# Kernel tuning notes

Measured on AMD Instinct MI355X. Metric: run time of the kernel, lower is better.

Reference implementation:

```python
import jax, jax.numpy as jnp
import numpy as np

D_MODEL = 1024
NUM_HEADS = 16
D_K = D_MODEL // NUM_HEADS
NEG_INF = -1e9


def setup_inputs() -> dict:
    key = jax.random.key(0)
    ks = jax.random.split(key, 9)
    B, S, D = 4, 2048, D_MODEL
    scale = 1.0 / np.sqrt(D)
    inp = {
        "x": jax.random.normal(ks[0], (B, S, D), dtype=jnp.float32),
        "Wq": jax.random.normal(ks[1], (D, D), dtype=jnp.float32) * scale,
        "bq": jnp.zeros((D,), dtype=jnp.float32),
        "Wk": jax.random.normal(ks[2], (D, D), dtype=jnp.float32) * scale,
        "bk": jnp.zeros((D,), dtype=jnp.float32),
        "Wv": jax.random.normal(ks[3], (D, D), dtype=jnp.float32) * scale,
        "bv": jnp.zeros((D,), dtype=jnp.float32),
        "Wo": jax.random.normal(ks[4], (D, D), dtype=jnp.float32) * scale,
        "bo": jnp.zeros((D,), dtype=jnp.float32),
    }
    return inp


def reference(x, Wq, bq, Wk, bk, Wv, bv, Wo, bo):
    B, S, D = x.shape
    H, dk = NUM_HEADS, D_K
    # padding mask: token is pad if any feature == 0; shape [B,1,1,S] (keys)
    mask = (x == 0).any(axis=-1)[:, None, None, :]

    def split_heads(t):  # [B,S,D] -> [B,H,S,dk]
        return t.reshape(B, S, H, dk).transpose(0, 2, 1, 3)

    q = split_heads(x @ Wq + bq)
    k = split_heads(x @ Wk + bk)
    v = split_heads(x @ Wv + bv)

    scores = jnp.einsum("bhqd,bhkd->bhqk", q, k) / np.sqrt(dk).astype(x.dtype)
    scores = jnp.where(mask, jnp.asarray(NEG_INF, x.dtype), scores)
    weights = jax.nn.softmax(scores, axis=-1)
    context = jnp.einsum("bhqk,bhkd->bhqd", weights, v)
    context = context.transpose(0, 2, 1, 3).reshape(B, S, D)
    return context @ Wo + bo
```

## Files before the change

### kernel.cpp

```cpp
#include <hip/hip_runtime.h>
#include <cstdint>
#include <cstddef>

static constexpr int Bz = 4, S = 2048, Dm = 1024, H = 16, DK = 64;
static constexpr int M = Bz * S;

typedef __attribute__((ext_vector_type(8))) short bf16x8;
typedef __attribute__((ext_vector_type(4))) float f32x4;

__device__ __forceinline__ unsigned short f2b(float f) {
    unsigned u = __float_as_uint(f);
    return (unsigned short)((u + 0x7FFFu + ((u >> 16) & 1u)) >> 16);
}

__device__ __forceinline__ unsigned cvtpk(float lo, float hi) {
    unsigned r;
    asm("v_cvt_pk_bf16_f32 %0, %1, %2" : "=v"(r) : "v"(lo), "v"(hi));
    return r;
}

__device__ __forceinline__ float fexp2(float x) {
#if __has_builtin(__builtin_amdgcn_exp2f)
    return __builtin_amdgcn_exp2f(x);
#else
    float r;
    asm("v_exp_f32 %0, %1" : "=v"(r) : "v"(x));
    return r;
#endif
}

__device__ __forceinline__ void gld_lds16(const void* g, void* l) {
    __builtin_amdgcn_global_load_lds(
        (const __attribute__((address_space(1))) unsigned int*)g,
        (__attribute__((address_space(3))) unsigned int*)l, 16, 0, 0);
}

__global__ __launch_bounds__(256) void k_conv(const float* __restrict__ x,
                                              const float* __restrict__ Wq, const float* __restrict__ Wk,
                                              const float* __restrict__ Wv, const float* __restrict__ Wo,
                                              unsigned short* __restrict__ xb,
                                              unsigned char* __restrict__ mask,
                                              unsigned short* __restrict__ Wt) {
    const int bid = blockIdx.x;
    const int tid = threadIdx.x;
    if (bid < M) {
        const int row = bid;
        const float4 v = *(const float4*)(x + (size_t)row * Dm + tid * 4);
        const bool z = (v.x == 0.f) | (v.y == 0.f) | (v.z == 0.f) | (v.w == 0.f);
        ushort4 o;
        o.x = f2b(v.x); o.y = f2b(v.y); o.z = f2b(v.z); o.w = f2b(v.w);
        *(ushort4*)(xb + (size_t)row * Dm + tid * 4) = o;
        __shared__ int zf;
        if (tid == 0) zf = 0;
        __syncthreads();
        if (z) zf = 1;
        __syncthreads();
        if (tid == 0) mask[row] = (unsigned char)zf;
    } else {
        const int wb = bid - M;
        const int zidx = wb >> 10;
        const int rem = wb & 1023;
        const int k0 = (rem & 31) * 32, n0 = (rem >> 5) * 32;
        const float* W = (zidx == 0) ? Wq : (zidx == 1) ? Wk : (zidx == 2) ? Wv : Wo;
        unsigned short* o = Wt + (size_t)zidx * Dm * Dm;
        __shared__ float tile[32][33];
        const int tx = tid & 31, ty = tid >> 5;
#pragma unroll
        for (int i = 0; i < 4; i++)
            tile[ty + 8 * i][tx] = W[(size_t)(k0 + ty + 8 * i) * Dm + n0 + tx];
        __syncthreads();
#pragma unroll
        for (int i = 0; i < 4; i++)
            o[(size_t)(n0 + ty + 8 * i) * Dm + k0 + tx] = f2b(tile[tx][ty + 8 * i]);
    }
}

template <int MODE>
__global__ __launch_bounds__(256) void k_gemm(
    const unsigned short* __restrict__ A,
    const unsigned short* __restrict__ Bw,
    const float* __restrict__ bias0, const float* __restrict__ bias1, const float* __restrict__ bias2,
    unsigned short* __restrict__ Qo, unsigned short* __restrict__ Ko,
    unsigned short* __restrict__ Vto, float* __restrict__ Co)
{
    __shared__ unsigned short sA[128 * 64];
    __shared__ unsigned short sB[128 * 64];
    const int m0 = blockIdx.x * 128;
    const int gn0 = blockIdx.y * 128;
    const int tid = threadIdx.x;
    const int lane = tid & 63;
    const int wid = tid >> 6;
    const int wm = wid & 1, wn = wid >> 1;
    const int lr = lane & 15;
    const int lg = lane >> 4;
    f32x4 acc[4][4] = {};
    const int csrc = ((lane & 7) ^ (lane >> 3)) << 4;
    const char* gA = (const char*)A + (size_t)(m0 + (tid >> 3)) * (Dm * 2) + csrc;
    const char* gB = (const char*)Bw + (size_t)(gn0 + (tid >> 3)) * (Dm * 2) + csrc;
    for (int k0 = 0; k0 < Dm; k0 += 64) {
        __syncthreads();
#pragma unroll
        for (int j = 0; j < 4; j++) {
            gld_lds16(gA + (size_t)(j * 32) * (Dm * 2) + k0 * 2, sA + j * 2048 + wid * 512);
            gld_lds16(gB + (size_t)(j * 32) * (Dm * 2) + k0 * 2, sB + j * 2048 + wid * 512);
        }
        __syncthreads();
#pragma unroll
        for (int h = 0; h < 2; h++) {
            bf16x8 af[4], bg[4];
#pragma unroll
            for (int mi = 0; mi < 4; mi++) {
                const int row = wm * 64 + mi * 16 + lr;
                af[mi] = *(const bf16x8*)((const char*)sA + row * 128 +
                                          (((h * 4 + lg) ^ (lr & 7)) << 4));
            }
#pragma unroll
            for (int ni = 0; ni < 4; ni++) {
                const int row = wn * 64 + ni * 16 + lr;
                bg[ni] = *(const bf16x8*)((const char*)sB + row * 128 +
                                          (((h * 4 + lg) ^ (lr & 7)) << 4));
            }
#pragma unroll
            for (int mi = 0; mi < 4; mi++)
#pragma unroll
                for (int ni = 0; ni < 4; ni++)
                    acc[mi][ni] = __builtin_amdgcn_mfma_f32_16x16x32_bf16(af[mi], bg[ni], acc[mi][ni], 0, 0, 0);
        }
    }
#pragma unroll
    for (int mi = 0; mi < 4; mi++) {
        const int row0 = m0 + wm * 64 + mi * 16 + lg * 4;
#pragma unroll
        for (int ni = 0; ni < 4; ni++) {
            const int gn = gn0 + wn * 64 + ni * 16 + lr;
            const int t = gn >> 10;
            const int n = gn & 1023;
            const int h = n >> 6, d = n & 63;
            const float bsv = (MODE == 0)
                ? ((t == 0) ? bias0[n] : (t == 1) ? bias1[n] : bias2[n])
                : bias0[gn];
#pragma unroll
            for (int r = 0; r < 4; r++) {
                const int row = row0 + r;
                const float v = acc[mi][ni][r] + bsv;
                if (MODE == 0) {
                    const int bb = row >> 11;
                    const int s = row & (S - 1);
                    const size_t bh = (size_t)bb * H + h;
                    if (t == 0) {
                        Qo[(bh * S + s) * DK + d] = f2b(v * 0.18033688011f);
                    } else if (t == 1) {
                        Ko[(bh * S + s) * DK + d] = f2b(v);
                    } else {
                        const int k5 = s & 31;
                        const int sp = (s & ~31) | ((k5 & 12) << 1) | ((k5 >> 4) << 2) | (k5 & 3);
                        Vto[(bh * DK + d) * S + sp] = f2b(v);
                    }
                } else {
                    Co[(size_t)row * Dm + gn] = v;
                }
            }
        }
    }
}

__global__ __launch_bounds__(256, 2) void k_attn(
    const unsigned short* __restrict__ Q, const unsigned short* __restrict__ K,
    const unsigned short* __restrict__ Vt, const unsigned char* __restrict__ mask,
    unsigned short* __restrict__ ctx)
{
    __shared__ unsigned short sK[2 * 2048];
    __shared__ unsigned short sV[2 * 2048];
    const int wg = blockIdx.x;
    const int sz = (wg & 7) * 128 + (wg >> 3);
    const int xt = sz & 15;
    const int bh = sz >> 4;
    const int bidx = bh >> 4, h = bh & 15;
    const int tid = threadIdx.x, lane = tid & 63, wid = tid >> 6;
    const int lr = lane & 15, lg = lane >> 4;
    const int qbase = xt * 128 + wid * 32;
    const size_t hoff = (size_t)bh * S * DK;
    const unsigned char* mrow = mask + bidx * S;
    const uint4 mza = *(const uint4*)(mrow + lane * 32);
    const uint4 mzb = *(const uint4*)(mrow + lane * 32 + 16);
    const bool anymask =
        __ballot((mza.x | mza.y | mza.z | mza.w | mzb.x | mzb.y | mzb.z | mzb.w) != 0) != 0ull;
    const unsigned short* qp = Q + hoff + (size_t)(qbase + lr) * DK;
    const bf16x8 aqA0 = *(const bf16x8*)(qp + lg * 8);
    const bf16x8 aqA1 = *(const bf16x8*)(qp + 32 + lg * 8);
    const bf16x8 aqB0 = *(const bf16x8*)(qp + 16 * DK + lg * 8);
    const bf16x8 aqB1 = *(const bf16x8*)(qp + 16 * DK + 32 + lg * 8);
    f32x4 oA[4] = {}, oB[4] = {};
    f32x4 lvA = {}, lvB = {};
    const int rwk = lane >> 3;
    const int csK = ((lane & 7) ^ rwk) << 4;
    const char* gK = (const char*)(K + hoff) + (size_t)(wid * 8 + rwk) * 128 + csK;
    const int rv = lane >> 2;
    const int csV = ((lane & 3) ^ ((rv >> 1) & 3)) << 4;
    const char* gV = (const char*)(Vt + hoff) + (size_t)(wid * 16 + rv) * (S * 2) + csV;
    constexpr int NT = S / 32;
    unsigned short* const wKd = sK + wid * 512;
    unsigned short* const wVd = sV + wid * 512;

    gld_lds16(gK, wKd);
    gld_lds16(gV, wVd);
    gK += 4096; gV += 64;

    auto body = [&](int t, const char* sKc, const char* sVc, int nbuf) {
        asm volatile("s_waitcnt vmcnt(0)" ::: "memory");
        __builtin_amdgcn_s_barrier();
        __builtin_amdgcn_sched_barrier(0);
        if (t + 1 < NT) {
            gld_lds16(gK, wKd + nbuf * 2048);
            gld_lds16(gV, wVd + nbuf * 2048);
            gK += 4096; gV += 64;
        }
        f32x4 zA[2], zB[2];
        __builtin_amdgcn_s_setprio(1);
#pragma unroll
        for (int nt = 0; nt < 2; nt++) {
            const int row = nt * 16 + lr;
            const int sw = (row & 7) << 4;
            const bf16x8 kf0 = *(const bf16x8*)(sKc + ((row * 128 + lg * 16) ^ sw));
            const bf16x8 kf1 = *(const bf16x8*)(sKc + ((row * 128 + 64 + lg * 16) ^ sw));
            f32x4 a = {};
            a = __builtin_amdgcn_mfma_f32_16x16x32_bf16(kf0, aqA0, a, 0, 0, 0);
            zA[nt] = __builtin_amdgcn_mfma_f32_16x16x32_bf16(kf1, aqA1, a, 0, 0, 0);
            f32x4 b = {};
            b = __builtin_amdgcn_mfma_f32_16x16x32_bf16(kf0, aqB0, b, 0, 0, 0);
            zB[nt] = __builtin_amdgcn_mfma_f32_16x16x32_bf16(kf1, aqB1, b, 0, 0, 0);
        }
        __builtin_amdgcn_s_setprio(0);
        if (anymask) {
            const unsigned long long bal =
                __ballot(mrow[t * 32 + (lane & 31)] != 0) & 0xFFFFFFFFull;
            if (bal) {
#pragma unroll
                for (int nt = 0; nt < 2; nt++)
#pragma unroll
                    for (int r = 0; r < 4; r++)
                        if ((bal >> (nt * 16 + lg * 4 + r)) & 1) { zA[nt][r] = -1e9f; zB[nt][r] = -1e9f; }
            }
        }
        union { unsigned u[4]; bf16x8 v; } wA0, wB0;
#pragma unroll
        for (int nt = 0; nt < 2; nt++) {
#pragma unroll
            for (int r = 0; r < 4; r++) zA[nt][r] = fexp2(zA[nt][r]);
            lvA += zA[nt];
        }
        wA0.u[0] = cvtpk(zA[0][0], zA[0][1]); wA0.u[1] = cvtpk(zA[0][2], zA[0][3]);
        wA0.u[2] = cvtpk(zA[1][0], zA[1][1]); wA0.u[3] = cvtpk(zA[1][2], zA[1][3]);
#pragma unroll
        for (int nt = 0; nt < 2; nt++) {
#pragma unroll
            for (int r = 0; r < 4; r++) zB[nt][r] = fexp2(zB[nt][r]);
            lvB += zB[nt];
        }
        wB0.u[0] = cvtpk(zB[0][0], zB[0][1]); wB0.u[1] = cvtpk(zB[0][2], zB[0][3]);
        wB0.u[2] = cvtpk(zB[1][0], zB[1][1]); wB0.u[3] = cvtpk(zB[1][2], zB[1][3]);
        __builtin_amdgcn_s_setprio(1);
#pragma unroll
        for (int dt = 0; dt < 4; dt++) {
            const int row = dt * 16 + lr;
            const int sw = (row >> 1) & 3;
            const bf16x8 v0 = *(const bf16x8*)(sVc + row * 64 + ((lg ^ sw) << 4));
            oA[dt] = __builtin_amdgcn_mfma_f32_16x16x32_bf16(wA0.v, v0, oA[dt], 0, 0, 0);
            oB[dt] = __builtin_amdgcn_mfma_f32_16x16x32_bf16(wB0.v, v0, oB[dt], 0, 0, 0);
        }
        __builtin_amdgcn_s_setprio(0);
        asm volatile("s_waitcnt lgkmcnt(0)" ::: "memory");
    };

    const char* const sKb0 = (const char*)sK;
    const char* const sKb1 = sKb0 + 4096;
    const char* const sVb0 = (const char*)sV;
    const char* const sVb1 = sVb0 + 4096;
    for (int t = 0; t < NT; t += 2) {
        body(t,     sKb0, sVb0, 1);
        body(t + 1, sKb1, sVb1, 0);
    }

    float lsA = (lvA[0] + lvA[1]) + (lvA[2] + lvA[3]);
    lsA += __shfl_xor(lsA, 16, 64);
    lsA += __shfl_xor(lsA, 32, 64);
    float lsB = (lvB[0] + lvB[1]) + (lvB[2] + lvB[3]);
    lsB += __shfl_xor(lsB, 16, 64);
    lsB += __shfl_xor(lsB, 32, 64);
#pragma unroll
    for (int r = 0; r < 4; r++) {
        const float iA = 1.f / __shfl(lsA, lg * 4 + r, 16);
        const float iB = 1.f / __shfl(lsB, lg * 4 + r, 16);
        const int sA_ = qbase + lg * 4 + r;
#pragma unroll
        for (int dt = 0; dt < 4; dt++) {
            const int col = h * 64 + dt * 16 + lr;
            ctx[((size_t)bidx * S + sA_) * Dm + col]      = f2b(oA[dt][r] * iA);
            ctx[((size_t)bidx * S + sA_ + 16) * Dm + col] = f2b(oB[dt][r] * iB);
        }
    }
}

extern "C" void kernel_launch(void* const* d_in, const int* in_sizes, int n_in,
                              void* d_out, int out_size, void* d_ws, size_t ws_size,
                              hipStream_t stream)
{
    (void)in_sizes; (void)n_in; (void)out_size; (void)ws_size;
    const float* x  = (const float*)d_in[0];
    const float* Wq = (const float*)d_in[1];
    const float* bq = (const float*)d_in[2];
    const float* Wk = (const float*)d_in[3];
    const float* bk = (const float*)d_in[4];
    const float* Wv = (const float*)d_in[5];
    const float* bv = (const float*)d_in[6];
    const float* Wo = (const float*)d_in[7];
    const float* bo = (const float*)d_in[8];
    float* out = (float*)d_out;
    char* ws = (char*)d_ws;
    unsigned short* xb  = (unsigned short*)(ws);
    unsigned short* Wt  = (unsigned short*)(ws + ((size_t)16 << 20));
    unsigned short* Qb  = (unsigned short*)(ws + ((size_t)24 << 20));
    unsigned short* Kb  = (unsigned short*)(ws + ((size_t)40 << 20));
    unsigned short* Vtb = (unsigned short*)(ws + ((size_t)56 << 20));
    unsigned short* ctx = (unsigned short*)(ws + ((size_t)72 << 20));
    unsigned char*  msk = (unsigned char*)(ws + ((size_t)88 << 20));

    k_conv<<<dim3(M + 4096), dim3(256), 0, stream>>>(x, Wq, Wk, Wv, Wo, xb, msk, Wt);
    k_gemm<0><<<dim3(M / 128, 3072 / 128), dim3(256), 0, stream>>>(
        xb, Wt, bq, bk, bv, Qb, Kb, Vtb, nullptr);
    k_attn<<<dim3(Bz * H * (S / 128)), dim3(256), 0, stream>>>(Qb, Kb, Vtb, msk, ctx);
    k_gemm<1><<<dim3(M / 128, 1024 / 128), dim3(256), 0, stream>>>(
        ctx, Wt + (size_t)3 * Dm * Dm, bo, nullptr, nullptr, nullptr, nullptr, nullptr, out);
}
```

Before: 197.2 us.

## Split QKV projection into dedicated 256x128-tile GEMM with 512 threads

After: 198.6 us. Within noise of the previous version (+0.7%).

```diff
diff --git a/kernel.cpp b/kernel.cpp
--- a/kernel.cpp
+++ b/kernel.cpp
@@ -75,13 +75,91 @@
     }
 }
 
-template <int MODE>
-__global__ __launch_bounds__(256) void k_gemm(
+__global__ __launch_bounds__(512, 2) void k_g0(
     const unsigned short* __restrict__ A,
     const unsigned short* __restrict__ Bw,
-    const float* __restrict__ bias0, const float* __restrict__ bias1, const float* __restrict__ bias2,
+    const float* __restrict__ bq, const float* __restrict__ bk, const float* __restrict__ bv,
     unsigned short* __restrict__ Qo, unsigned short* __restrict__ Ko,
-    unsigned short* __restrict__ Vto, float* __restrict__ Co)
+    unsigned short* __restrict__ Vto)
+{
+    __shared__ unsigned short sA[256 * 32];
+    __shared__ unsigned short sB[128 * 32];
+    const int m0 = blockIdx.x * 256;
+    const int n0 = blockIdx.y * 128;
+    const int tid = threadIdx.x;
+    const int lane = tid & 63;
+    const int wid = tid >> 6;
+    const int wm = wid >> 1;
+    const int wn = wid & 1;
+    const int lr = lane & 15, lg = lane >> 4;
+    f32x4 acc[4][4] = {};
+    const int srow = tid >> 2;
+    const int csrc = ((lane & 3) ^ ((lane >> 2) & 3)) << 4;
+    const char* gA = (const char*)A + (size_t)(m0 + srow) * (Dm * 2) + csrc;
+    const char* gB = (const char*)Bw + (size_t)(n0 + srow) * (Dm * 2) + csrc;
+    unsigned short* const dA = sA + wid * 512;
+    unsigned short* const dB = sB + wid * 512;
+    for (int kb = 0; kb < Dm * 2; kb += 64) {
+        __syncthreads();
+        gld_lds16(gA + kb, dA);
+        gld_lds16(gA + (size_t)128 * (Dm * 2) + kb, dA + 4096);
+        gld_lds16(gB + kb, dB);
+        __syncthreads();
+        bf16x8 af[4], bg[4];
+#pragma unroll
+        for (int mi = 0; mi < 4; mi++) {
+            const int row = wm * 64 + mi * 16 + lr;
+            af[mi] = *(const bf16x8*)((const char*)sA + row * 64 + ((lg ^ (row & 3)) << 4));
+        }
+#pragma unroll
+        for (int ni = 0; ni < 4; ni++) {
+            const int row = wn * 64 + ni * 16 + lr;
+            bg[ni] = *(const bf16x8*)((const char*)sB + row * 64 + ((lg ^ (row & 3)) << 4));
+        }
+        __builtin_amdgcn_s_setprio(1);
+#pragma unroll
+        for (int mi = 0; mi < 4; mi++)
+#pragma unroll
+            for (int ni = 0; ni < 4; ni++)
+                acc[mi][ni] = __builtin_amdgcn_mfma_f32_16x16x32_bf16(af[mi], bg[ni], acc[mi][ni], 0, 0, 0);
+        __builtin_amdgcn_s_setprio(0);
+    }
+#pragma unroll
+    for (int mi = 0; mi < 4; mi++) {
+        const int row0 = m0 + wm * 64 + mi * 16 + lg * 4;
+#pragma unroll
+        for (int ni = 0; ni < 4; ni++) {
+            const int gn = n0 + wn * 64 + ni * 16 + lr;
+            const int t = gn >> 10;
+            const int n = gn & 1023;
+            const int h = n >> 6, d = n & 63;
+            const float bsv = (t == 0) ? bq[n] : (t == 1) ? bk[n] : bv[n];
+#pragma unroll
+            for (int r = 0; r < 4; r++) {
+                const int row = row0 + r;
+                const float v = acc[mi][ni][r] + bsv;
+                const int bb = row >> 11;
+                const int s = row & (S - 1);
+                const size_t bh = (size_t)bb * H + h;
+                if (t == 0) {
+                    Qo[(bh * S + s) * DK + d] = f2b(v * 0.18033688011f);
+                } else if (t == 1) {
+                    Ko[(bh * S + s) * DK + d] = f2b(v);
+                } else {
+                    const int k5 = s & 31;
+                    const int sp = (s & ~31) | ((k5 & 12) << 1) | ((k5 >> 4) << 2) | (k5 & 3);
+                    Vto[(bh * DK + d) * S + sp] = f2b(v);
+                }
+            }
+        }
+    }
+}
+
+__global__ __launch_bounds__(256) void k_g1(
+    const unsigned short* __restrict__ A,
+    const unsigned short* __restrict__ Bw,
+    const float* __restrict__ bias0,
+    float* __restrict__ Co)
 {
     __shared__ unsigned short sA[128 * 64];
     __shared__ unsigned short sB[128 * 64];
@@ -133,33 +211,10 @@
 #pragma unroll
         for (int ni = 0; ni < 4; ni++) {
             const int gn = gn0 + wn * 64 + ni * 16 + lr;
-            const int t = gn >> 10;
-            const int n = gn & 1023;
-            const int h = n >> 6, d = n & 63;
-            const float bsv = (MODE == 0)
-                ? ((t == 0) ? bias0[n] : (t == 1) ? bias1[n] : bias2[n])
-                : bias0[gn];
-#pragma unroll
-            for (int r = 0; r < 4; r++) {
-                const int row = row0 + r;
-                const float v = acc[mi][ni][r] + bsv;
-                if (MODE == 0) {
-                    const int bb = row >> 11;
-                    const int s = row & (S - 1);
-                    const size_t bh = (size_t)bb * H + h;
-                    if (t == 0) {
-                        Qo[(bh * S + s) * DK + d] = f2b(v * 0.18033688011f);
-                    } else if (t == 1) {
-                        Ko[(bh * S + s) * DK + d] = f2b(v);
-                    } else {
-                        const int k5 = s & 31;
-                        const int sp = (s & ~31) | ((k5 & 12) << 1) | ((k5 >> 4) << 2) | (k5 & 3);
-                        Vto[(bh * DK + d) * S + sp] = f2b(v);
-                    }
-                } else {
-                    Co[(size_t)row * Dm + gn] = v;
-                }
-            }
+            const float bsv = bias0[gn];
+#pragma unroll
+            for (int r = 0; r < 4; r++)
+                Co[(size_t)(row0 + r) * Dm + gn] = acc[mi][ni][r] + bsv;
         }
     }
 }
@@ -326,9 +381,9 @@
     unsigned char*  msk = (unsigned char*)(ws + ((size_t)88 << 20));
 
     k_conv<<<dim3(M + 4096), dim3(256), 0, stream>>>(x, Wq, Wk, Wv, Wo, xb, msk, Wt);
-    k_gemm<0><<<dim3(M / 128, 3072 / 128), dim3(256), 0, stream>>>(
-        xb, Wt, bq, bk, bv, Qb, Kb, Vtb, nullptr);
+    k_g0<<<dim3(M / 256, 3072 / 128), dim3(512), 0, stream>>>(
+        xb, Wt, bq, bk, bv, Qb, Kb, Vtb);
     k_attn<<<dim3(Bz * H * (S / 128)), dim3(256), 0, stream>>>(Qb, Kb, Vtb, msk, ctx);
-    k_gemm<1><<<dim3(M / 128, 1024 / 128), dim3(256), 0, stream>>>(
-        ctx, Wt + (size_t)3 * Dm * Dm, bo, nullptr, nullptr, nullptr, nullptr, nullptr, out);
-}
+    k_g1<<<dim3(M / 128, 1024 / 128), dim3(256), 0, stream>>>(
+        ctx, Wt + (size_t)3 * Dm * Dm, bo, out);
+}
```
